# Kernel tuning notes

Measured on AMD Instinct MI355X. Metric: run time of the kernel, lower is better.

The kernel has to match this reference:

```python
import jax, jax.numpy as jnp
import numpy as np

B, S, D, H = 4, 2048, 1024, 16
DK = D // H


def setup_inputs() -> dict:
    key = jax.random.key(0)
    ks = jax.random.split(key, 11)
    std = 1.0 / np.sqrt(D)
    mk = lambda k: jax.random.uniform(k, (D, D), jnp.float32, -std, std)
    mb = lambda k: jax.random.uniform(k, (D,), jnp.float32, -std, std)
    return {
        "query": jax.random.normal(ks[0], (B, S, D), jnp.float32),
        "key": jax.random.normal(ks[1], (B, S, D), jnp.float32),
        "value": jax.random.normal(ks[2], (B, S, D), jnp.float32),
        "Wq": mk(ks[3]), "bq": mb(ks[4]),
        "Wk": mk(ks[5]), "bk": mb(ks[6]),
        "Wv": mk(ks[7]), "bv": mb(ks[8]),
        "Wo": mk(ks[9]), "bo": mb(ks[10]),
    }


def reference(query, key, value, Wq, bq, Wk, bk, Wv, bv, Wo, bo):
    # Linear projections (torch Linear: x @ W.T + b)
    Q = query @ Wq.T + bq   # [B,S,D]
    K = key @ Wk.T + bk
    V = value @ Wv.T + bv
    # split heads -> [B,H,S,DK]
    Q = Q.reshape(B, S, H, DK).transpose(0, 2, 1, 3)
    K = K.reshape(B, S, H, DK).transpose(0, 2, 1, 3)
    V = V.reshape(B, S, H, DK).transpose(0, 2, 1, 3)
    scale = 1.0 / jnp.sqrt(jnp.asarray(DK, Q.dtype))
    scores = jnp.einsum("bhqd,bhkd->bhqk", Q, K) * scale  # [B,H,S,S]
    attn = jax.nn.softmax(scores, axis=-1)
    out = jnp.einsum("bhqk,bhkd->bhqd", attn, V)          # [B,H,S,DK]
    out = out.transpose(0, 2, 1, 3).reshape(B, S, D)       # [B,S,D]
    return out @ Wo.T + bo
```

## Files before the change

### kernel.cpp

```cpp
#include <hip/hip_runtime.h>
#include <hip/hip_bf16.h>
#include <stdint.h>


using f32x4  = __attribute__((ext_vector_type(4))) float;
using f32x16 = __attribute__((ext_vector_type(16))) float;
using s16x8  = __attribute__((ext_vector_type(8))) short;
using u16x8  = __attribute__((ext_vector_type(8))) unsigned short;
using u16x4  = __attribute__((ext_vector_type(4))) unsigned short;

#define MFMA16(a, b, c) __builtin_amdgcn_mfma_f32_16x16x32_bf16((a), (b), (c), 0, 0, 0)
#define MFMA32(a, b, c) __builtin_amdgcn_mfma_f32_32x32x16_bf16((a), (b), (c), 0, 0, 0)

#define GLL16(gptr, lptr)                                                      \
  __builtin_amdgcn_global_load_lds(                                            \
      (const __attribute__((address_space(1))) void*)(gptr),                   \
      (__attribute__((address_space(3))) void*)(lptr), 16, 0, 0)

__device__ __forceinline__ unsigned short f2bf(float f) {
  union { __hip_bfloat16 h; unsigned short u; } cv;
  cv.h = __float2bfloat16(f);
  return cv.u;
}

__device__ __forceinline__ unsigned int pkrne(float a, float b) {
  unsigned int ua = __builtin_bit_cast(unsigned int, a);
  unsigned int ub = __builtin_bit_cast(unsigned int, b);
  ua = ua + 0x7FFFu + ((ua >> 16) & 1u);
  ub = ub + 0x7FFFu + ((ub >> 16) & 1u);
  return (ua >> 16) | (ub & 0xFFFF0000u);
}

__device__ __forceinline__ float exp2a(float x) {
  return __builtin_amdgcn_exp2f(x);
}

__device__ __forceinline__ s16x8 pack8(const float4& a, const float4& b) {
  uint4 u;
  u.x = pkrne(a.x, a.y); u.y = pkrne(a.z, a.w);
  u.z = pkrne(b.x, b.y); u.w = pkrne(b.z, b.w);
  return *reinterpret_cast<const s16x8*>(&u);
}

__global__ __launch_bounds__(256) void cast_w_kernel(
    const float* __restrict__ wq, const float* __restrict__ wk,
    const float* __restrict__ wv, const float* __restrict__ wo,
    unsigned short* __restrict__ dst) {
  int i = blockIdx.x * 256 + threadIdx.x;
  int m = i >> 18;
  int off = i & 0x3FFFF;
  const float* src = (m == 0) ? wq : (m == 1) ? wk : (m == 2) ? wv : wo;
  float4 v = reinterpret_cast<const float4*>(src)[off];
  u16x4 o;
  o[0] = f2bf(v.x); o[1] = f2bf(v.y); o[2] = f2bf(v.z); o[3] = f2bf(v.w);
  *reinterpret_cast<u16x4*>(dst + (size_t)i * 4) = o;
}

__global__ __launch_bounds__(256) void gemm_qkv_kernel(
    const float* __restrict__ xq, const float* __restrict__ xk, const float* __restrict__ xv,
    const unsigned short* __restrict__ wbf,
    const float* __restrict__ bq, const float* __restrict__ bk, const float* __restrict__ bv,
    unsigned short* __restrict__ Qh, unsigned short* __restrict__ Kh,
    unsigned short* __restrict__ Vh) {
  const int z = blockIdx.z;
  const float* X = (z == 0) ? xq : (z == 1) ? xk : xv;
  const float* bias = (z == 0) ? bq : (z == 1) ? bk : bv;
  const unsigned short* W = wbf + (size_t)z * 1048576;
  unsigned short* dst = (z == 0) ? Qh : (z == 1) ? Kh : Vh;
  const float qscale = (z == 0) ? 0.18033688011112042f : 1.0f;

  __shared__ __align__(16) float Af[128 * 32];
  __shared__ __align__(16) unsigned short Bs[128 * 32];

  const int t = threadIdx.x;
  const int lane = t & 63, w = t >> 6;
  const int g = lane >> 4, c = lane & 15;
  const int wm = (w >> 1) * 64, wn = (w & 1) * 64;
  const int n0 = (blockIdx.y & 7) * 128;
  const int m0 = (blockIdx.x * 8 + (blockIdx.y >> 3)) * 128;

  f32x4 acc[4][4];
#pragma unroll
  for (int i = 0; i < 4; i++)
#pragma unroll
    for (int j = 0; j < 4; j++) acc[i][j] = (f32x4)0.0f;

  const int ar = lane >> 3;
  const int acs = (lane & 7) ^ ar;
  const int br_ = lane >> 2;
  const int bcs = (lane & 3) ^ (br_ & 3);

  for (int k0 = 0; k0 < 1024; k0 += 32) {
    __syncthreads();
#pragma unroll
    for (int i = 0; i < 4; i++) {
      int ii = w * 4 + i;
      const float* gsrc = X + (size_t)(m0 + ii * 8 + ar) * 1024 + k0 + acs * 4;
      GLL16(gsrc, &Af[ii * 256]);
    }
#pragma unroll
    for (int i = 0; i < 2; i++) {
      int ii = w * 2 + i;
      const unsigned short* gsrc = W + (size_t)(n0 + ii * 16 + br_) * 1024 + k0 + bcs * 8;
      GLL16(gsrc, &Bs[ii * 512]);
    }
    __syncthreads();

    s16x8 af[4], bfr[4];
#pragma unroll
    for (int mt = 0; mt < 4; mt++) {
      int r = wm + mt * 16 + c;
      int x = r & 7;
      const float* rowp = &Af[r * 32];
      float4 f0 = *reinterpret_cast<const float4*>(rowp + (((g * 2) ^ x) << 2));
      float4 f1 = *reinterpret_cast<const float4*>(rowp + (((g * 2 + 1) ^ x) << 2));
      af[mt] = pack8(f0, f1);
    }
#pragma unroll
    for (int nt = 0; nt < 4; nt++) {
      int r = wn + nt * 16 + c;
      bfr[nt] = *reinterpret_cast<const s16x8*>(&Bs[r * 32 + ((g ^ (r & 3)) << 3)]);
    }
#pragma unroll
    for (int mt = 0; mt < 4; mt++)
#pragma unroll
      for (int nt = 0; nt < 4; nt++)
        acc[mt][nt] = MFMA16(af[mt], bfr[nt], acc[mt][nt]);
  }

#pragma unroll
  for (int mt = 0; mt < 4; mt++)
#pragma unroll
    for (int nt = 0; nt < 4; nt++) {
      int n = n0 + wn + nt * 16 + c;
      float bb = bias[n];
      int h = n >> 6, dk = n & 63;
#pragma unroll
      for (int r = 0; r < 4; r++) {
        int m = m0 + wm + mt * 16 + g * 4 + r;
        int b = m >> 11, s = m & 2047;
        dst[(((size_t)b * 16 + h) * 2048 + s) * 64 + dk] =
            f2bf((acc[mt][nt][r] + bb) * qscale);
      }
    }
}

__global__ __launch_bounds__(256) void gemm_out_kernel(
    const unsigned short* __restrict__ AO, const unsigned short* __restrict__ Wo,
    const float* __restrict__ bo, float* __restrict__ out) {
  __shared__ __align__(16) unsigned short Asm_[128 * 32];
  __shared__ __align__(16) unsigned short Bsm_[128 * 32];

  const int t = threadIdx.x;
  const int lane = t & 63, w = t >> 6;
  const int g = lane >> 4, c = lane & 15;
  const int wm = (w >> 1) * 64, wn = (w & 1) * 64;
  const int n0 = (blockIdx.y & 7) * 128;
  const int m0 = (blockIdx.x * 8 + (blockIdx.y >> 3)) * 128;

  f32x4 acc[4][4];
#pragma unroll
  for (int i = 0; i < 4; i++)
#pragma unroll
    for (int j = 0; j < 4; j++) acc[i][j] = (f32x4)0.0f;

  const int br_ = lane >> 2;
  const int bcs = (lane & 3) ^ (br_ & 3);

  for (int k0 = 0; k0 < 1024; k0 += 32) {
    __syncthreads();
#pragma unroll
    for (int i = 0; i < 2; i++) {
      int ii = w * 2 + i;
      const unsigned short* ga = AO + (size_t)(m0 + ii * 16 + br_) * 1024 + k0 + bcs * 8;
      GLL16(ga, &Asm_[ii * 512]);
      const unsigned short* gb = Wo + (size_t)(n0 + ii * 16 + br_) * 1024 + k0 + bcs * 8;
      GLL16(gb, &Bsm_[ii * 512]);
    }
    __syncthreads();

    s16x8 af[4], bfr[4];
#pragma unroll
    for (int mt = 0; mt < 4; mt++) {
      int r = wm + mt * 16 + c;
      af[mt] = *reinterpret_cast<const s16x8*>(&Asm_[r * 32 + ((g ^ (r & 3)) << 3)]);
    }
#pragma unroll
    for (int nt = 0; nt < 4; nt++) {
      int r = wn + nt * 16 + c;
      bfr[nt] = *reinterpret_cast<const s16x8*>(&Bsm_[r * 32 + ((g ^ (r & 3)) << 3)]);
    }
#pragma unroll
    for (int mt = 0; mt < 4; mt++)
#pragma unroll
      for (int nt = 0; nt < 4; nt++)
        acc[mt][nt] = MFMA16(af[mt], bfr[nt], acc[mt][nt]);
  }

#pragma unroll
  for (int mt = 0; mt < 4; mt++)
#pragma unroll
    for (int nt = 0; nt < 4; nt++) {
      int n = n0 + wn + nt * 16 + c;
      float bb = bo[n];
#pragma unroll
      for (int r = 0; r < 4; r++) {
        int m = m0 + wm + mt * 16 + g * 4 + r;
        out[(size_t)m * 1024 + n] = acc[mt][nt][r] + bb;
      }
    }
}

__global__ __launch_bounds__(512) void attn_kernel(
    const unsigned short* __restrict__ Qh, const unsigned short* __restrict__ Kh,
    const unsigned short* __restrict__ Vh, unsigned short* __restrict__ AO) {
  const int bh = blockIdx.x * 8 + (blockIdx.y >> 3);
  const int b = bh >> 4, h = bh & 15;
  const int q0 = (blockIdx.y & 7) * 256;
  const int t = threadIdx.x, lane = t & 63, w = t >> 6;
  const int lo = lane & 31, hi = lane >> 5;

  __shared__ __align__(16) unsigned short Ks[2][64 * 64];
  __shared__ __align__(16) unsigned short Vt[2][64 * 64];

  const size_t kvbase = (size_t)bh * 2048 * 64;

  s16x8 qb[4];
  {
    const unsigned short* qp = Qh + kvbase + (size_t)(q0 + w * 32 + lo) * 64;
#pragma unroll
    for (int ks = 0; ks < 4; ks++)
      qb[ks] = *reinterpret_cast<const s16x8*>(qp + ks * 16 + hi * 8);
  }

  f32x16 oacc[2];
  oacc[0] = (f32x16)0.0f; oacc[1] = (f32x16)0.0f;
  float lsum = 0.0f;

  const int skrow = t >> 3, sks = t & 7;
  const int kgc = sks ^ (skrow & 7) ^ w;
  const int vkrow = t >> 3, vd0 = (t & 7) * 8;
  const int vwc = w ^ (t & 7);
  const int vcl = vkrow & 7;

  const int rx0 = (lo & 7) ^ (lo >> 3);
  const int rx1 = (lo & 7) ^ (4 | (lo >> 3));

  uint4 kk, vv;
  kk = *reinterpret_cast<const uint4*>(Kh + kvbase + (size_t)skrow * 64 + kgc * 8);
  vv = *reinterpret_cast<const uint4*>(Vh + kvbase + (size_t)vkrow * 64 + vd0);
  *reinterpret_cast<uint4*>(&Ks[0][(size_t)t * 8]) = kk;
  {
    const unsigned short* vs = reinterpret_cast<const unsigned short*>(&vv);
#pragma unroll
    for (int j = 0; j < 8; j++)
      Vt[0][(vd0 + j) * 64 + ((vwc ^ j) << 3) + vcl] = vs[j];
  }

  for (int it = 0; it < 32; ++it) {
    const int cur = it & 1, nxt = cur ^ 1;
    const bool more = (it < 31);
    if (more) {
      const int kv = (it + 1) * 64;
      kk = *reinterpret_cast<const uint4*>(Kh + kvbase + (size_t)(kv + skrow) * 64 + kgc * 8);
      vv = *reinterpret_cast<const uint4*>(Vh + kvbase + (size_t)(kv + vkrow) * 64 + vd0);
    }
    __syncthreads();

    f32x16 st[2];
    st[0] = (f32x16)0.0f; st[1] = (f32x16)0.0f;
#pragma unroll
    for (int kb = 0; kb < 2; kb++) {
      const int rx = kb ? rx1 : rx0;
#pragma unroll
      for (int ks = 0; ks < 4; ks++) {
        s16x8 ka = *reinterpret_cast<const s16x8*>(
            &Ks[cur][(kb * 32 + lo) * 64 + (((ks * 2 + hi) ^ rx) << 3)]);
        st[kb] = MFMA32(ka, qb[ks], st[kb]);
      }
    }

    s16x8 pa[4];
    float s0 = 0.0f, s1 = 0.0f, s2 = 0.0f, s3 = 0.0f;
#pragma unroll
    for (int kb = 0; kb < 2; kb++) {
      float e[16];
#pragma unroll
      for (int r = 0; r < 16; r += 4) {
        e[r]     = exp2a(st[kb][r]);
        e[r + 1] = exp2a(st[kb][r + 1]);
        e[r + 2] = exp2a(st[kb][r + 2]);
        e[r + 3] = exp2a(st[kb][r + 3]);
        s0 += e[r]; s1 += e[r + 1]; s2 += e[r + 2]; s3 += e[r + 3];
      }
#pragma unroll
      for (int half = 0; half < 2; half++) {
        const float* eb = e + half * 8;
        unsigned int x1 = pkrne(eb[0], eb[1]);
        unsigned int x2 = pkrne(eb[2], eb[3]);
        unsigned int y1 = pkrne(eb[4], eb[5]);
        unsigned int y2 = pkrne(eb[6], eb[7]);
        asm volatile("v_permlane32_swap_b32 %0, %1" : "+v"(x1), "+v"(y1));
        asm volatile("v_permlane32_swap_b32 %0, %1" : "+v"(x2), "+v"(y2));
        uint4 u;
        u.x = x1; u.y = x2; u.z = y1; u.w = y2;
        pa[kb * 2 + half] = *reinterpret_cast<const s16x8*>(&u);
      }
    }
    lsum += (s0 + s1) + (s2 + s3);

    if (more) {
      *reinterpret_cast<uint4*>(&Ks[nxt][(size_t)t * 8]) = kk;
      const unsigned short* vs = reinterpret_cast<const unsigned short*>(&vv);
#pragma unroll
      for (int j = 0; j < 8; j++)
        Vt[nxt][(vd0 + j) * 64 + ((vwc ^ j) << 3) + vcl] = vs[j];
    }

#pragma unroll
    for (int ks = 0; ks < 4; ks++)
#pragma unroll
      for (int db = 0; db < 2; db++) {
        const int rx = db ? rx1 : rx0;
        s16x8 vb = *reinterpret_cast<const s16x8*>(
            &Vt[cur][(db * 32 + lo) * 64 + (((ks * 2 + hi) ^ rx) << 3)]);
        oacc[db] = MFMA32(pa[ks], vb, oacc[db]);
      }
  }

  float ltot = lsum + __shfl_xor(lsum, 32);
  float linv = 1.0f / ltot;
#pragma unroll
  for (int r = 0; r < 16; r++) {
    int qr = (r & 3) + ((r >> 2) << 3) + (hi << 2);
    float inv_r = __shfl(linv, qr);
    int srow = q0 + w * 32 + qr;
    size_t obase = ((size_t)b * 2048 + srow) * 1024 + (size_t)h * 64;
    AO[obase + lo]      = f2bf(oacc[0][r] * inv_r);
    AO[obase + 32 + lo] = f2bf(oacc[1][r] * inv_r);
  }
}

extern "C" void kernel_launch(void* const* d_in, const int* in_sizes, int n_in,
                              void* d_out, int out_size, void* d_ws, size_t ws_size,
                              hipStream_t stream) {
  const float* query = (const float*)d_in[0];
  const float* key   = (const float*)d_in[1];
  const float* value = (const float*)d_in[2];
  const float* Wq = (const float*)d_in[3];
  const float* bq = (const float*)d_in[4];
  const float* Wk = (const float*)d_in[5];
  const float* bk = (const float*)d_in[6];
  const float* Wv = (const float*)d_in[7];
  const float* bv = (const float*)d_in[8];
  const float* Wo = (const float*)d_in[9];
  const float* bo = (const float*)d_in[10];

  uint8_t* wsb = (uint8_t*)d_ws;
  unsigned short* wbf = (unsigned short*)wsb;
  unsigned short* Qh  = (unsigned short*)(wsb + 8388608);
  unsigned short* Kh  = (unsigned short*)(wsb + 8388608 + 16777216);
  unsigned short* Vh  = (unsigned short*)(wsb + 8388608 + 2 * 16777216);
  unsigned short* AO  = (unsigned short*)(wsb + 8388608 + 3 * 16777216);

  cast_w_kernel<<<dim3(4096), dim3(256), 0, stream>>>(Wq, Wk, Wv, Wo, wbf);
  gemm_qkv_kernel<<<dim3(8, 64, 3), dim3(256), 0, stream>>>(
      query, key, value, wbf, bq, bk, bv, Qh, Kh, Vh);
  attn_kernel<<<dim3(8, 64), dim3(512), 0, stream>>>(Qh, Kh, Vh, AO);
  gemm_out_kernel<<<dim3(8, 64), dim3(256), 0, stream>>>(
      AO, wbf + (size_t)3 * 1048576, bo, (float*)d_out);
}
```

Measured before the change: 235.8 us.

## Double GEMM K-tile to 64 and convert activations to bf16 before LDS

```diff
diff --git a/kernel.cpp b/kernel.cpp
--- a/kernel.cpp
+++ b/kernel.cpp
@@ -33,13 +33,6 @@
 
 __device__ __forceinline__ float exp2a(float x) {
   return __builtin_amdgcn_exp2f(x);
-}
-
-__device__ __forceinline__ s16x8 pack8(const float4& a, const float4& b) {
-  uint4 u;
-  u.x = pkrne(a.x, a.y); u.y = pkrne(a.z, a.w);
-  u.z = pkrne(b.x, b.y); u.w = pkrne(b.z, b.w);
-  return *reinterpret_cast<const s16x8*>(&u);
 }
 
 __global__ __launch_bounds__(256) void cast_w_kernel(
@@ -69,8 +62,8 @@
   unsigned short* dst = (z == 0) ? Qh : (z == 1) ? Kh : Vh;
   const float qscale = (z == 0) ? 0.18033688011112042f : 1.0f;
 
-  __shared__ __align__(16) float Af[128 * 32];
-  __shared__ __align__(16) unsigned short Bs[128 * 32];
+  __shared__ __align__(16) unsigned short Ab[128 * 64];
+  __shared__ __align__(16) unsigned short Bs[128 * 64];
 
   const int t = threadIdx.x;
   const int lane = t & 63, w = t >> 6;
@@ -85,47 +78,53 @@
 #pragma unroll
     for (int j = 0; j < 4; j++) acc[i][j] = (f32x4)0.0f;
 
-  const int ar = lane >> 3;
-  const int acs = (lane & 7) ^ ar;
-  const int br_ = lane >> 2;
-  const int bcs = (lane & 3) ^ (br_ & 3);
-
-  for (int k0 = 0; k0 < 1024; k0 += 32) {
+  const int arow_lo = t >> 4;
+  const int af0 = (t & 15) * 4;
+  const int alc = (t & 15) >> 1;
+  const int ah = (t & 15) & 1;
+  const int blr = lane >> 3;
+  const int bgc = (lane & 7) ^ blr;
+
+  for (int kt = 0; kt < 16; ++kt) {
+    const int k0 = kt * 64;
     __syncthreads();
 #pragma unroll
     for (int i = 0; i < 4; i++) {
       int ii = w * 4 + i;
-      const float* gsrc = X + (size_t)(m0 + ii * 8 + ar) * 1024 + k0 + acs * 4;
-      GLL16(gsrc, &Af[ii * 256]);
-    }
-#pragma unroll
-    for (int i = 0; i < 2; i++) {
-      int ii = w * 2 + i;
-      const unsigned short* gsrc = W + (size_t)(n0 + ii * 16 + br_) * 1024 + k0 + bcs * 8;
+      const unsigned short* gsrc = W + (size_t)(n0 + ii * 8 + blr) * 1024 + k0 + bgc * 8;
       GLL16(gsrc, &Bs[ii * 512]);
     }
-    __syncthreads();
-
-    s16x8 af[4], bfr[4];
-#pragma unroll
-    for (int mt = 0; mt < 4; mt++) {
-      int r = wm + mt * 16 + c;
-      int x = r & 7;
-      const float* rowp = &Af[r * 32];
-      float4 f0 = *reinterpret_cast<const float4*>(rowp + (((g * 2) ^ x) << 2));
-      float4 f1 = *reinterpret_cast<const float4*>(rowp + (((g * 2 + 1) ^ x) << 2));
-      af[mt] = pack8(f0, f1);
-    }
-#pragma unroll
-    for (int nt = 0; nt < 4; nt++) {
-      int r = wn + nt * 16 + c;
-      bfr[nt] = *reinterpret_cast<const s16x8*>(&Bs[r * 32 + ((g ^ (r & 3)) << 3)]);
-    }
-#pragma unroll
-    for (int mt = 0; mt < 4; mt++)
-#pragma unroll
-      for (int nt = 0; nt < 4; nt++)
-        acc[mt][nt] = MFMA16(af[mt], bfr[nt], acc[mt][nt]);
+#pragma unroll
+    for (int j = 0; j < 8; j++) {
+      int r = j * 16 + arow_lo;
+      float4 v = *reinterpret_cast<const float4*>(X + (size_t)(m0 + r) * 1024 + k0 + af0);
+      uint2 p;
+      p.x = pkrne(v.x, v.y);
+      p.y = pkrne(v.z, v.w);
+      int pc = alc ^ (r & 7);
+      *reinterpret_cast<uint2*>(&Ab[r * 64 + pc * 8 + ah * 4]) = p;
+    }
+    __syncthreads();
+
+#pragma unroll
+    for (int ks = 0; ks < 2; ks++) {
+      s16x8 af[4], bfr[4];
+#pragma unroll
+      for (int mt = 0; mt < 4; mt++) {
+        int r = wm + mt * 16 + c;
+        af[mt] = *reinterpret_cast<const s16x8*>(&Ab[r * 64 + (((ks * 4 + g) ^ (c & 7)) << 3)]);
+      }
+#pragma unroll
+      for (int nt = 0; nt < 4; nt++) {
+        int r = wn + nt * 16 + c;
+        bfr[nt] = *reinterpret_cast<const s16x8*>(&Bs[r * 64 + (((ks * 4 + g) ^ (c & 7)) << 3)]);
+      }
+#pragma unroll
+      for (int mt = 0; mt < 4; mt++)
+#pragma unroll
+        for (int nt = 0; nt < 4; nt++)
+          acc[mt][nt] = MFMA16(af[mt], bfr[nt], acc[mt][nt]);
+    }
   }
 
 #pragma unroll
@@ -148,8 +147,8 @@
 __global__ __launch_bounds__(256) void gemm_out_kernel(
     const unsigned short* __restrict__ AO, const unsigned short* __restrict__ Wo,
     const float* __restrict__ bo, float* __restrict__ out) {
-  __shared__ __align__(16) unsigned short Asm_[128 * 32];
-  __shared__ __align__(16) unsigned short Bsm_[128 * 32];
+  __shared__ __align__(16) unsigned short Asm_[128 * 64];
+  __shared__ __align__(16) unsigned short Bsm_[128 * 64];
 
   const int t = threadIdx.x;
   const int lane = t & 63, w = t >> 6;
@@ -164,37 +163,41 @@
 #pragma unroll
     for (int j = 0; j < 4; j++) acc[i][j] = (f32x4)0.0f;
 
-  const int br_ = lane >> 2;
-  const int bcs = (lane & 3) ^ (br_ & 3);
-
-  for (int k0 = 0; k0 < 1024; k0 += 32) {
-    __syncthreads();
-#pragma unroll
-    for (int i = 0; i < 2; i++) {
-      int ii = w * 2 + i;
-      const unsigned short* ga = AO + (size_t)(m0 + ii * 16 + br_) * 1024 + k0 + bcs * 8;
+  const int blr = lane >> 3;
+  const int bgc = (lane & 7) ^ blr;
+
+  for (int kt = 0; kt < 16; ++kt) {
+    const int k0 = kt * 64;
+    __syncthreads();
+#pragma unroll
+    for (int i = 0; i < 4; i++) {
+      int ii = w * 4 + i;
+      const unsigned short* ga = AO + (size_t)(m0 + ii * 8 + blr) * 1024 + k0 + bgc * 8;
       GLL16(ga, &Asm_[ii * 512]);
-      const unsigned short* gb = Wo + (size_t)(n0 + ii * 16 + br_) * 1024 + k0 + bcs * 8;
+      const unsigned short* gb = Wo + (size_t)(n0 + ii * 8 + blr) * 1024 + k0 + bgc * 8;
       GLL16(gb, &Bsm_[ii * 512]);
     }
     __syncthreads();
 
-    s16x8 af[4], bfr[4];
-#pragma unroll
-    for (int mt = 0; mt < 4; mt++) {
-      int r = wm + mt * 16 + c;
-      af[mt] = *reinterpret_cast<const s16x8*>(&Asm_[r * 32 + ((g ^ (r & 3)) << 3)]);
-    }
-#pragma unroll
-    for (int nt = 0; nt < 4; nt++) {
-      int r = wn + nt * 16 + c;
-      bfr[nt] = *reinterpret_cast<const s16x8*>(&Bsm_[r * 32 + ((g ^ (r & 3)) << 3)]);
-    }
-#pragma unroll
-    for (int mt = 0; mt < 4; mt++)
-#pragma unroll
-      for (int nt = 0; nt < 4; nt++)
-        acc[mt][nt] = MFMA16(af[mt], bfr[nt], acc[mt][nt]);
+#pragma unroll
+    for (int ks = 0; ks < 2; ks++) {
+      s16x8 af[4], bfr[4];
+#pragma unroll
+      for (int mt = 0; mt < 4; mt++) {
+        int r = wm + mt * 16 + c;
+        af[mt] = *reinterpret_cast<const s16x8*>(&Asm_[r * 64 + (((ks * 4 + g) ^ (c & 7)) << 3)]);
+      }
+#pragma unroll
+      for (int nt = 0; nt < 4; nt++) {
+        int r = wn + nt * 16 + c;
+        bfr[nt] = *reinterpret_cast<const s16x8*>(&Bsm_[r * 64 + (((ks * 4 + g) ^ (c & 7)) << 3)]);
+      }
+#pragma unroll
+      for (int mt = 0; mt < 4; mt++)
+#pragma unroll
+        for (int nt = 0; nt < 4; nt++)
+          acc[mt][nt] = MFMA16(af[mt], bfr[nt], acc[mt][nt]);
+    }
   }
 
 #pragma unroll
```

After: 218.9 us. 1.08x faster.

## Double-buffer GEMM tiles and stage fp32 activations as bf16 in LDS

Applied to the files above, without the earlier changes.

```diff
diff --git a/kernel.cpp b/kernel.cpp
--- a/kernel.cpp
+++ b/kernel.cpp
@@ -33,13 +33,6 @@
 
 __device__ __forceinline__ float exp2a(float x) {
   return __builtin_amdgcn_exp2f(x);
-}
-
-__device__ __forceinline__ s16x8 pack8(const float4& a, const float4& b) {
-  uint4 u;
-  u.x = pkrne(a.x, a.y); u.y = pkrne(a.z, a.w);
-  u.z = pkrne(b.x, b.y); u.w = pkrne(b.z, b.w);
-  return *reinterpret_cast<const s16x8*>(&u);
 }
 
 __global__ __launch_bounds__(256) void cast_w_kernel(
@@ -69,8 +62,8 @@
   unsigned short* dst = (z == 0) ? Qh : (z == 1) ? Kh : Vh;
   const float qscale = (z == 0) ? 0.18033688011112042f : 1.0f;
 
-  __shared__ __align__(16) float Af[128 * 32];
-  __shared__ __align__(16) unsigned short Bs[128 * 32];
+  __shared__ __align__(16) unsigned short Ab[2][128 * 32];
+  __shared__ __align__(16) unsigned short Bs[2][128 * 32];
 
   const int t = threadIdx.x;
   const int lane = t & 63, w = t >> 6;
@@ -85,47 +78,69 @@
 #pragma unroll
     for (int j = 0; j < 4; j++) acc[i][j] = (f32x4)0.0f;
 
-  const int ar = lane >> 3;
-  const int acs = (lane & 7) ^ ar;
-  const int br_ = lane >> 2;
-  const int bcs = (lane & 3) ^ (br_ & 3);
-
-  for (int k0 = 0; k0 < 1024; k0 += 32) {
-    __syncthreads();
-#pragma unroll
-    for (int i = 0; i < 4; i++) {
-      int ii = w * 4 + i;
-      const float* gsrc = X + (size_t)(m0 + ii * 8 + ar) * 1024 + k0 + acs * 4;
-      GLL16(gsrc, &Af[ii * 256]);
-    }
+  const int ar2 = t >> 1, ah2 = t & 1;
+  const float* Arow = X + (size_t)(m0 + ar2) * 1024 + ah2 * 16;
+  const int apc0 = ((ah2 * 2) ^ (ar2 & 3)) * 8;
+  const int apc1 = ((ah2 * 2 + 1) ^ (ar2 & 3)) * 8;
+  const int blr = lane >> 2;
+  const int bgc = (lane & 3) ^ (blr & 3);
+
+  float4 a0, a1, a2, a3;
+
+  auto loadA = [&](int k0) {
+    const float4* p = reinterpret_cast<const float4*>(Arow + k0);
+    a0 = p[0]; a1 = p[1]; a2 = p[2]; a3 = p[3];
+  };
+  auto writeA = [&](int buf) {
+    uint4 q0, q1;
+    q0.x = pkrne(a0.x, a0.y); q0.y = pkrne(a0.z, a0.w);
+    q0.z = pkrne(a1.x, a1.y); q0.w = pkrne(a1.z, a1.w);
+    q1.x = pkrne(a2.x, a2.y); q1.y = pkrne(a2.z, a2.w);
+    q1.z = pkrne(a3.x, a3.y); q1.w = pkrne(a3.z, a3.w);
+    *reinterpret_cast<uint4*>(&Ab[buf][ar2 * 32 + apc0]) = q0;
+    *reinterpret_cast<uint4*>(&Ab[buf][ar2 * 32 + apc1]) = q1;
+  };
+  auto stageB = [&](int buf, int k0) {
 #pragma unroll
     for (int i = 0; i < 2; i++) {
       int ii = w * 2 + i;
-      const unsigned short* gsrc = W + (size_t)(n0 + ii * 16 + br_) * 1024 + k0 + bcs * 8;
-      GLL16(gsrc, &Bs[ii * 512]);
-    }
-    __syncthreads();
+      const unsigned short* gsrc = W + (size_t)(n0 + ii * 16 + blr) * 1024 + k0 + bgc * 8;
+      GLL16(gsrc, &Bs[buf][ii * 512]);
+    }
+  };
+
+  loadA(0);
+  stageB(0, 0);
+  writeA(0);
+  __syncthreads();
+
+  for (int kt = 0; kt < 32; ++kt) {
+    const int cur = kt & 1, nxt = cur ^ 1;
+    const bool more = (kt < 31);
+    if (more) {
+      loadA((kt + 1) * 32);
+      stageB(nxt, (kt + 1) * 32);
+    }
 
     s16x8 af[4], bfr[4];
 #pragma unroll
     for (int mt = 0; mt < 4; mt++) {
       int r = wm + mt * 16 + c;
-      int x = r & 7;
-      const float* rowp = &Af[r * 32];
-      float4 f0 = *reinterpret_cast<const float4*>(rowp + (((g * 2) ^ x) << 2));
-      float4 f1 = *reinterpret_cast<const float4*>(rowp + (((g * 2 + 1) ^ x) << 2));
-      af[mt] = pack8(f0, f1);
+      af[mt] = *reinterpret_cast<const s16x8*>(&Ab[cur][r * 32 + ((g ^ (r & 3)) << 3)]);
     }
 #pragma unroll
     for (int nt = 0; nt < 4; nt++) {
       int r = wn + nt * 16 + c;
-      bfr[nt] = *reinterpret_cast<const s16x8*>(&Bs[r * 32 + ((g ^ (r & 3)) << 3)]);
+      bfr[nt] = *reinterpret_cast<const s16x8*>(&Bs[cur][r * 32 + ((g ^ (r & 3)) << 3)]);
     }
 #pragma unroll
     for (int mt = 0; mt < 4; mt++)
 #pragma unroll
       for (int nt = 0; nt < 4; nt++)
         acc[mt][nt] = MFMA16(af[mt], bfr[nt], acc[mt][nt]);
+
+    if (more) writeA(nxt);
+    __syncthreads();
   }
 
 #pragma unroll
@@ -148,8 +163,8 @@
 __global__ __launch_bounds__(256) void gemm_out_kernel(
     const unsigned short* __restrict__ AO, const unsigned short* __restrict__ Wo,
     const float* __restrict__ bo, float* __restrict__ out) {
-  __shared__ __align__(16) unsigned short Asm_[128 * 32];
-  __shared__ __align__(16) unsigned short Bsm_[128 * 32];
+  __shared__ __align__(16) unsigned short Asm_[2][128 * 32];
+  __shared__ __align__(16) unsigned short Bsm_[2][128 * 32];
 
   const int t = threadIdx.x;
   const int lane = t & 63, w = t >> 6;
@@ -164,37 +179,45 @@
 #pragma unroll
     for (int j = 0; j < 4; j++) acc[i][j] = (f32x4)0.0f;
 
-  const int br_ = lane >> 2;
-  const int bcs = (lane & 3) ^ (br_ & 3);
-
-  for (int k0 = 0; k0 < 1024; k0 += 32) {
-    __syncthreads();
+  const int blr = lane >> 2;
+  const int bgc = (lane & 3) ^ (blr & 3);
+
+  auto stage = [&](int buf, int k0) {
 #pragma unroll
     for (int i = 0; i < 2; i++) {
       int ii = w * 2 + i;
-      const unsigned short* ga = AO + (size_t)(m0 + ii * 16 + br_) * 1024 + k0 + bcs * 8;
-      GLL16(ga, &Asm_[ii * 512]);
-      const unsigned short* gb = Wo + (size_t)(n0 + ii * 16 + br_) * 1024 + k0 + bcs * 8;
-      GLL16(gb, &Bsm_[ii * 512]);
-    }
-    __syncthreads();
+      const unsigned short* ga = AO + (size_t)(m0 + ii * 16 + blr) * 1024 + k0 + bgc * 8;
+      GLL16(ga, &Asm_[buf][ii * 512]);
+      const unsigned short* gb = Wo + (size_t)(n0 + ii * 16 + blr) * 1024 + k0 + bgc * 8;
+      GLL16(gb, &Bsm_[buf][ii * 512]);
+    }
+  };
+
+  stage(0, 0);
+  __syncthreads();
+
+  for (int kt = 0; kt < 32; ++kt) {
+    const int cur = kt & 1, nxt = cur ^ 1;
+    if (kt < 31) stage(nxt, (kt + 1) * 32);
 
     s16x8 af[4], bfr[4];
 #pragma unroll
     for (int mt = 0; mt < 4; mt++) {
       int r = wm + mt * 16 + c;
-      af[mt] = *reinterpret_cast<const s16x8*>(&Asm_[r * 32 + ((g ^ (r & 3)) << 3)]);
+      af[mt] = *reinterpret_cast<const s16x8*>(&Asm_[cur][r * 32 + ((g ^ (r & 3)) << 3)]);
     }
 #pragma unroll
     for (int nt = 0; nt < 4; nt++) {
       int r = wn + nt * 16 + c;
-      bfr[nt] = *reinterpret_cast<const s16x8*>(&Bsm_[r * 32 + ((g ^ (r & 3)) << 3)]);
+      bfr[nt] = *reinterpret_cast<const s16x8*>(&Bsm_[cur][r * 32 + ((g ^ (r & 3)) << 3)]);
     }
 #pragma unroll
     for (int mt = 0; mt < 4; mt++)
 #pragma unroll
       for (int nt = 0; nt < 4; nt++)
         acc[mt][nt] = MFMA16(af[mt], bfr[nt], acc[mt][nt]);
+
+    __syncthreads();
   }
 
 #pragma unroll
```

Measured after the change: 229.3 us. 2.7% less time.
